# Optimization experiments

Hardware: AMD Instinct MI355X
Metric: run time of the kernel (lower is better)

Reference implementation:

```python
import jax, jax.numpy as jnp
import numpy as np
from jax.scipy.special import erf

N = 100000
PATCH = 10           # cells per dim: covers 2*nsigma*sigma_max / spacing <= 9
SPACING = (0.5, 0.5, 0.5)
NSIGMA = 3.0


def setup_inputs() -> dict:
    key = jax.random.key(0)
    k1, k2, k3, k4 = jax.random.split(key, 4)
    # sigma in [0.25, 0.75] distance units = [0.5, 1.5] x grid spacing
    sigma = 0.25 + 0.5 * jax.random.uniform(k1, (N, 3), dtype=jnp.float32)
    time = jax.random.uniform(k2, (N,), dtype=jnp.float32) * 10.0
    charge = jax.random.uniform(k3, (N,), dtype=jnp.float32) * 1000.0
    tail = jax.random.normal(k4, (N, 3), dtype=jnp.float32) * 20.0
    grid_spacing = jnp.asarray(SPACING, dtype=jnp.float32)
    nsigma = jnp.asarray(NSIGMA, dtype=jnp.float32)
    return {"sigma": sigma, "time": time, "charge": charge, "tail": tail,
            "grid_spacing": grid_spacing, "nsigma": nsigma}


def _transform(point, time):
    # pdims=(1,2), tdim=-1: new = [point[:,1], point[:,2], time]
    return jnp.stack([point[:, 1], point[:, 2], time], axis=-1)


def _raster_depos(grid_spacing, center, sigma, charge, nsigma):
    # center, sigma: [N,3]; returns rasters [N,P,P,P], offsets [N,3] int32
    imin = jnp.floor((center - nsigma * sigma) / grid_spacing)   # [N,3]
    offsets = imin.astype(jnp.int32)
    k = jnp.arange(PATCH + 1, dtype=center.dtype)                # cell edges index
    edges = (imin[:, :, None] + k) * grid_spacing[None, :, None]  # [N,3,P+1]
    z = (edges - center[:, :, None]) / (jnp.sqrt(2.0).astype(center.dtype) * sigma[:, :, None])
    cdf = 0.5 * (1.0 + erf(z))                                   # [N,3,P+1]
    w = cdf[..., 1:] - cdf[..., :-1]                             # [N,3,P] per-dim cell integrals
    rasters = (charge[:, None, None, None]
               * w[:, 0, :, None, None]
               * w[:, 1, None, :, None]
               * w[:, 2, None, None, :])                         # [N,P,P,P]
    return rasters, offsets


def reference(sigma, time, charge, tail, grid_spacing, nsigma):
    center = _transform(tail, time)
    rasters, offsets = _raster_depos(grid_spacing, center, sigma, charge, nsigma)
    return rasters, offsets
```

## Files before the change

kernel.cpp:

```cpp
#include <hip/hip_runtime.h>
#include <hip/hip_bf16.h>

#define PATCH 10
#define CELLS 1000
#define DPB   16

__global__ __launch_bounds__(512) void raster_kernel(
    const float* __restrict__ sigma,
    const float* __restrict__ time,
    const float* __restrict__ charge,
    const float* __restrict__ tail,
    const float* __restrict__ gs,
    const float* __restrict__ nsig,
    float* __restrict__ out_r,
    float* __restrict__ out_off,
    int n)
{
    const int d0  = blockIdx.x * DPB;
    const int tid = threadIdx.x;

    __shared__ float wq[DPB][32];

    if (tid < DPB * 30) {
        const int d   = tid / 30;
        const int r   = tid - d * 30;
        const int dim = r / 10;
        const int k   = r - dim * 10;
        const int depo = d0 + d;
        if (depo < n) {
            float c;
            if (dim == 0)      c = tail[depo * 3 + 1];
            else if (dim == 1) c = tail[depo * 3 + 2];
            else               c = time[depo];
            const float sg = sigma[depo * 3 + dim];
            const float sp = gs[dim];
            const float ns = nsig[0];
            const float imin = floorf((c - ns * sg) / sp);
            const float inv  = 1.0f / (1.41421356237309f * sg);
            const float e0 = (imin + (float)k) * sp;
            const float cdf0 = 0.5f * (1.0f + erff((e0 - c) * inv));
            const float cdf1 = 0.5f * (1.0f + erff((e0 + sp - c) * inv));
            wq[d][dim * 10 + k] = cdf1 - cdf0;
            if (k == 0) {
                out_off[(size_t)depo * 3 + dim] = (float)(int)imin;
                if (dim == 0) wq[d][30] = charge[depo];
            }
        }
    }
    __syncthreads();

    if (tid < 500) {
        const int half = (tid >= 250) ? 1 : 0;
        const int c4   = tid - 250 * half;
        const int cell0 = c4 * 4;

        int a0[4], a1[4], a2[4];
#pragma unroll
        for (int c = 0; c < 4; ++c) {
            const int cell = cell0 + c;
            a0[c] = cell / 100;
            a1[c] = 10 + (cell / 10) % 10;
            a2[c] = 20 + cell % 10;
        }

#pragma unroll
        for (int it = 0; it < DPB / 2; ++it) {
            const int d    = it * 2 + half;
            const int depo = d0 + d;
            if (depo < n) {
                const float q = wq[d][30];
                float4 v;
                v.x = q * wq[d][a0[0]] * wq[d][a1[0]] * wq[d][a2[0]];
                v.y = q * wq[d][a0[1]] * wq[d][a1[1]] * wq[d][a2[1]];
                v.z = q * wq[d][a0[2]] * wq[d][a1[2]] * wq[d][a2[2]];
                v.w = q * wq[d][a0[3]] * wq[d][a1[3]] * wq[d][a2[3]];
                float4* dst = reinterpret_cast<float4*>(out_r + (size_t)depo * CELLS) + c4;
                *dst = v;
            }
        }
    }
}

extern "C" void kernel_launch(void* const* d_in, const int* in_sizes, int n_in,
                              void* d_out, int out_size, void* d_ws, size_t ws_size,
                              hipStream_t stream) {
    const float* sigma  = (const float*)d_in[0];
    const float* time_  = (const float*)d_in[1];
    const float* charge = (const float*)d_in[2];
    const float* tail   = (const float*)d_in[3];
    const float* gs     = (const float*)d_in[4];
    const float* nsig   = (const float*)d_in[5];

    const int n = in_sizes[1];

    float* out_r   = (float*)d_out;
    float* out_off = (float*)d_out + (size_t)n * CELLS;

    const int grid = (n + DPB - 1) / DPB;
    raster_kernel<<<grid, 512, 0, stream>>>(sigma, time_, charge, tail, gs, nsig,
                                            out_r, out_off, n);
}
```

Before: 84.74 us.

## Split per-dim weight computation into separate kernel via workspace

Moves the erf-based per-dimension weight computation into its own kernel that writes to a workspace buffer. A second kernel then only loads those weights into shared memory and streams the 400 MB raster output. The aim is to keep the erf math out of the store-bound kernel so it stays purely bandwidth-limited. This adds a second launch and a workspace round trip, and keeps the original fused kernel as a fallback when the workspace is too small.

```diff
diff --git a/kernel.cpp b/kernel.cpp
--- a/kernel.cpp
+++ b/kernel.cpp
@@ -1,52 +1,60 @@
 #include <hip/hip_runtime.h>
 #include <hip/hip_bf16.h>
 
-#define PATCH 10
 #define CELLS 1000
 #define DPB   16
+#define WSTRIDE 32
 
-__global__ __launch_bounds__(512) void raster_kernel(
+__global__ __launch_bounds__(256) void compute_w_kernel(
     const float* __restrict__ sigma,
     const float* __restrict__ time,
     const float* __restrict__ charge,
     const float* __restrict__ tail,
     const float* __restrict__ gs,
     const float* __restrict__ nsig,
+    float* __restrict__ out_off,
+    float* __restrict__ ws,
+    int n)
+{
+    const int idx = blockIdx.x * blockDim.x + threadIdx.x;
+    if (idx >= n * 30) return;
+    const int depo = idx / 30;
+    const int r    = idx - depo * 30;
+    const int dim  = r / 10;
+    const int k    = r - dim * 10;
+
+    float c;
+    if (dim == 0)      c = tail[depo * 3 + 1];
+    else if (dim == 1) c = tail[depo * 3 + 2];
+    else               c = time[depo];
+    const float sg   = sigma[depo * 3 + dim];
+    const float sp   = gs[dim];
+    const float ns   = nsig[0];
+    const float imin = floorf((c - ns * sg) / sp);
+    const float inv  = 1.0f / (1.41421356237309f * sg);
+    const float e0   = (imin + (float)k) * sp;
+    const float cdf0 = 0.5f * (1.0f + erff((e0 - c) * inv));
+    const float cdf1 = 0.5f * (1.0f + erff((e0 + sp - c) * inv));
+    ws[depo * WSTRIDE + dim * 10 + k] = cdf1 - cdf0;
+    if (k == 0) {
+        out_off[(size_t)depo * 3 + dim] = (float)(int)imin;
+        if (dim == 0) ws[depo * WSTRIDE + 30] = charge[depo];
+    }
+}
+
+__global__ __launch_bounds__(512) void store_kernel(
+    const float* __restrict__ ws,
     float* __restrict__ out_r,
-    float* __restrict__ out_off,
     int n)
 {
     const int d0  = blockIdx.x * DPB;
     const int tid = threadIdx.x;
 
-    __shared__ float wq[DPB][32];
+    __shared__ float wq[DPB][WSTRIDE];
 
-    if (tid < DPB * 30) {
-        const int d   = tid / 30;
-        const int r   = tid - d * 30;
-        const int dim = r / 10;
-        const int k   = r - dim * 10;
-        const int depo = d0 + d;
-        if (depo < n) {
-            float c;
-            if (dim == 0)      c = tail[depo * 3 + 1];
-            else if (dim == 1) c = tail[depo * 3 + 2];
-            else               c = time[depo];
-            const float sg = sigma[depo * 3 + dim];
-            const float sp = gs[dim];
-            const float ns = nsig[0];
-            const float imin = floorf((c - ns * sg) / sp);
-            const float inv  = 1.0f / (1.41421356237309f * sg);
-            const float e0 = (imin + (float)k) * sp;
-            const float cdf0 = 0.5f * (1.0f + erff((e0 - c) * inv));
-            const float cdf1 = 0.5f * (1.0f + erff((e0 + sp - c) * inv));
-            wq[d][dim * 10 + k] = cdf1 - cdf0;
-            if (k == 0) {
-                out_off[(size_t)depo * 3 + dim] = (float)(int)imin;
-                if (dim == 0) wq[d][30] = charge[depo];
-            }
-        }
-    }
+    const int lin = d0 * WSTRIDE + tid;
+    if (lin < n * WSTRIDE)
+        wq[tid >> 5][tid & 31] = ws[lin];
     __syncthreads();
 
     if (tid < 500) {
@@ -81,6 +89,73 @@
     }
 }
 
+__global__ __launch_bounds__(512) void raster_fused_kernel(
+    const float* __restrict__ sigma, const float* __restrict__ time,
+    const float* __restrict__ charge, const float* __restrict__ tail,
+    const float* __restrict__ gs, const float* __restrict__ nsig,
+    float* __restrict__ out_r, float* __restrict__ out_off, int n)
+{
+    const int d0  = blockIdx.x * DPB;
+    const int tid = threadIdx.x;
+    __shared__ float wq[DPB][32];
+
+    if (tid < DPB * 30) {
+        const int d   = tid / 30;
+        const int r   = tid - d * 30;
+        const int dim = r / 10;
+        const int k   = r - dim * 10;
+        const int depo = d0 + d;
+        if (depo < n) {
+            float c;
+            if (dim == 0)      c = tail[depo * 3 + 1];
+            else if (dim == 1) c = tail[depo * 3 + 2];
+            else               c = time[depo];
+            const float sg = sigma[depo * 3 + dim];
+            const float sp = gs[dim];
+            const float ns = nsig[0];
+            const float imin = floorf((c - ns * sg) / sp);
+            const float inv  = 1.0f / (1.41421356237309f * sg);
+            const float e0 = (imin + (float)k) * sp;
+            const float cdf0 = 0.5f * (1.0f + erff((e0 - c) * inv));
+            const float cdf1 = 0.5f * (1.0f + erff((e0 + sp - c) * inv));
+            wq[d][dim * 10 + k] = cdf1 - cdf0;
+            if (k == 0) {
+                out_off[(size_t)depo * 3 + dim] = (float)(int)imin;
+                if (dim == 0) wq[d][30] = charge[depo];
+            }
+        }
+    }
+    __syncthreads();
+
+    if (tid < 500) {
+        const int half = (tid >= 250) ? 1 : 0;
+        const int c4   = tid - 250 * half;
+        int a0[4], a1[4], a2[4];
+#pragma unroll
+        for (int c = 0; c < 4; ++c) {
+            const int cell = c4 * 4 + c;
+            a0[c] = cell / 100;
+            a1[c] = 10 + (cell / 10) % 10;
+            a2[c] = 20 + cell % 10;
+        }
+#pragma unroll
+        for (int it = 0; it < DPB / 2; ++it) {
+            const int d    = it * 2 + half;
+            const int depo = d0 + d;
+            if (depo < n) {
+                const float q = wq[d][30];
+                float4 v;
+                v.x = q * wq[d][a0[0]] * wq[d][a1[0]] * wq[d][a2[0]];
+                v.y = q * wq[d][a0[1]] * wq[d][a1[1]] * wq[d][a2[1]];
+                v.z = q * wq[d][a0[2]] * wq[d][a1[2]] * wq[d][a2[2]];
+                v.w = q * wq[d][a0[3]] * wq[d][a1[3]] * wq[d][a2[3]];
+                float4* dst = reinterpret_cast<float4*>(out_r + (size_t)depo * CELLS) + c4;
+                *dst = v;
+            }
+        }
+    }
+}
+
 extern "C" void kernel_launch(void* const* d_in, const int* in_sizes, int n_in,
                               void* d_out, int out_size, void* d_ws, size_t ws_size,
                               hipStream_t stream) {
@@ -96,7 +171,17 @@
     float* out_r   = (float*)d_out;
     float* out_off = (float*)d_out + (size_t)n * CELLS;
 
-    const int grid = (n + DPB - 1) / DPB;
-    raster_kernel<<<grid, 512, 0, stream>>>(sigma, time_, charge, tail, gs, nsig,
-                                            out_r, out_off, n);
+    const size_t ws_needed = (size_t)n * WSTRIDE * sizeof(float);
+    if (ws_size >= ws_needed) {
+        float* ws = (float*)d_ws;
+        const int ta = n * 30;
+        compute_w_kernel<<<(ta + 255) / 256, 256, 0, stream>>>(
+            sigma, time_, charge, tail, gs, nsig, out_off, ws, n);
+        const int grid = (n + DPB - 1) / DPB;
+        store_kernel<<<grid, 512, 0, stream>>>(ws, out_r, n);
+    } else {
+        const int grid = (n + DPB - 1) / DPB;
+        raster_fused_kernel<<<grid, 512, 0, stream>>>(
+            sigma, time_, charge, tail, gs, nsig, out_r, out_off, n);
+    }
 }
```

Result: slower. 97.88 us (+15.5%).
